# Kernel optimization log

Measured on AMD Instinct MI355X. Metric: run time of the kernel, lower is better.

The kernel has to match this reference:

```python
import jax, jax.numpy as jnp
import numpy as np

B, C_MAX, T = 128, 272, 512
D1 = 320
NUM_SUBJECTS = 8
NUM_CHANNELS = [272, 256, 240, 224, 208, 270, 260, 248]


def setup_inputs() -> dict:
    key = jax.random.key(0)
    k_x, k_w, k_s = jax.random.split(key, 3)
    X = jax.random.normal(k_x, (B, C_MAX, T), dtype=jnp.float32)
    subject_idxs = jax.random.randint(k_s, (B,), 0, NUM_SUBJECTS)
    # Per-subject Conv1d(kernel=1, bias=False) weights, padded to C_MAX.
    # Original module only reads the first num_channels[s] input channels;
    # zeroing the padded columns reproduces that exactly.
    W = jax.random.normal(k_w, (NUM_SUBJECTS, D1, C_MAX), dtype=jnp.float32) * 0.02
    mask = np.zeros((NUM_SUBJECTS, 1, C_MAX), dtype=np.float32)
    for s, nc in enumerate(NUM_CHANNELS):
        mask[s, 0, :nc] = 1.0
    W = W * jnp.asarray(mask)
    return {"X": X, "subject_idxs": subject_idxs, "W": W}


def reference(X, subject_idxs, W):
    # Gather per-sample weight matrix [B, D1, C_MAX] by subject id, then
    # batched 1x1 conv == matmul over channels at every time step.
    Wsel = W[subject_idxs]                      # [B, D1, C]
    out = jnp.einsum("bdc,bct->bdt", Wsel, X)   # [B, D1, T]
    return out
```

## Files before the change

### kernel.cpp

```cpp
#include <hip/hip_runtime.h>

#define BB    128
#define CC    272
#define TT    512
#define DD1   320
#define KC    32
#define NCHUNK 9
#define NT    64
#define MT    160
#define LDA   40
#define LDB2  66

typedef float  f32x4  __attribute__((ext_vector_type(4)));
typedef __bf16 bf16x4 __attribute__((ext_vector_type(4)));
typedef __bf16 bf16x8 __attribute__((ext_vector_type(8)));

#define BAR() asm volatile("s_waitcnt lgkmcnt(0)\ns_barrier" ::: "memory")

__global__ __launch_bounds__(256, 4)
void subj_conv_mfma(const float* __restrict__ X,
                    const int*   __restrict__ sidx,
                    const float* __restrict__ W,
                    float*       __restrict__ out) {
    const int b  = blockIdx.x;
    const int T0 = blockIdx.y * NT;
    const int d0 = blockIdx.z * MT;
    const int s  = sidx[b];

    __shared__ __bf16 As[2][MT * LDA];
    __shared__ float  Bs[2][KC * LDB2];

    const int tid  = threadIdx.x;
    const int lane = tid & 63;
    const int wv   = tid >> 6;
    const int wm   = wv & 1;
    const int wn   = wv >> 1;
    const int quad = lane >> 4;
    const int l16  = lane & 15;

    const float* Wb = W + ((size_t)s * DD1 + d0) * CC;
    const float* Xb = X + (size_t)b * CC * TT + T0;

    const int am  = tid >> 3;
    const int akk = (tid & 7) * 4;
    const int bcr = tid >> 4;
    const int bt  = (tid & 15) * 4;

    f32x4 acc[5][2];
#pragma unroll
    for (int mt = 0; mt < 5; ++mt) {
        acc[mt][0] = (f32x4){0.f, 0.f, 0.f, 0.f};
        acc[mt][1] = (f32x4){0.f, 0.f, 0.f, 0.f};
    }

    float4 pa[5];
    float4 pb[2];

    auto load_chunk = [&](int c0) {
#pragma unroll
        for (int p = 0; p < 5; ++p) {
            const int m = am + 32 * p;
            const int c = c0 + akk;
            float4 v = make_float4(0.f, 0.f, 0.f, 0.f);
            if (c < CC) v = *(const float4*)(Wb + (size_t)m * CC + c);
            pa[p] = v;
        }
#pragma unroll
        for (int p = 0; p < 2; ++p) {
            const int c = c0 + bcr + 16 * p;
            float4 v = make_float4(0.f, 0.f, 0.f, 0.f);
            if (c < CC) v = *(const float4*)(Xb + (size_t)c * TT + bt);
            pb[p] = v;
        }
    };

    auto store_chunk = [&](int buf) {
#pragma unroll
        for (int p = 0; p < 5; ++p) {
            const int m = am + 32 * p;
            bf16x4 h = {(__bf16)pa[p].x, (__bf16)pa[p].y,
                        (__bf16)pa[p].z, (__bf16)pa[p].w};
            *(bf16x4*)&As[buf][m * LDA + akk] = h;
        }
#pragma unroll
        for (int p = 0; p < 2; ++p) {
            const int cr = bcr + 16 * p;
            float* row = &Bs[buf][cr * LDB2 + bt];
            *(float2*)(row + 0) = make_float2(pb[p].x, pb[p].y);
            *(float2*)(row + 2) = make_float2(pb[p].z, pb[p].w);
        }
    };

    load_chunk(0);
    store_chunk(0);
    load_chunk(KC);
    BAR();

    for (int kc = 0; kc < NCHUNK; ++kc) {
        const int cur = kc & 1;

        bf16x8 bfr[2];
#pragma unroll
        for (int nt = 0; nt < 2; ++nt) {
            const int tcol = wn * 32 + nt * 16 + l16;
            bf16x8 h;
#pragma unroll
            for (int j = 0; j < 8; ++j)
                h[j] = (__bf16)Bs[cur][(quad * 8 + j) * LDB2 + tcol];
            bfr[nt] = h;
        }

#pragma unroll
        for (int mt = 0; mt < 5; ++mt) {
            bf16x8 af = *(const bf16x8*)&As[cur][(wm * 80 + mt * 16 + l16) * LDA + quad * 8];
#pragma unroll
            for (int nt = 0; nt < 2; ++nt)
                acc[mt][nt] = __builtin_amdgcn_mfma_f32_16x16x32_bf16(
                    af, bfr[nt], acc[mt][nt], 0, 0, 0);
        }

        if (kc + 1 < NCHUNK) {
            store_chunk(1 - cur);
            if (kc + 2 < NCHUNK) load_chunk((kc + 2) * KC);
            BAR();
        }
    }

#pragma unroll
    for (int mt = 0; mt < 5; ++mt) {
        const int d = d0 + wm * 80 + mt * 16 + quad * 4;
#pragma unroll
        for (int nt = 0; nt < 2; ++nt) {
            float* ob = out + ((size_t)b * DD1 + d) * TT + T0 + wn * 32 + nt * 16 + l16;
#pragma unroll
            for (int r = 0; r < 4; ++r)
                ob[(size_t)r * TT] = acc[mt][nt][r];
        }
    }
}

extern "C" void kernel_launch(void* const* d_in, const int* in_sizes, int n_in,
                              void* d_out, int out_size, void* d_ws, size_t ws_size,
                              hipStream_t stream) {
    const float* X    = (const float*)d_in[0];
    const int*   sidx = (const int*)  d_in[1];
    const float* W    = (const float*)d_in[2];
    float*       out  = (float*)d_out;

    dim3 grid(BB, TT / NT, 2);
    dim3 block(256);
    subj_conv_mfma<<<grid, block, 0, stream>>>(X, sidx, W, out);
}
```

Measured before the change: 164.5 us.

## Store X tile transposed as bf16 in LDS for vector fragment reads

```diff
diff --git a/kernel.cpp b/kernel.cpp
--- a/kernel.cpp
+++ b/kernel.cpp
@@ -9,7 +9,7 @@
 #define NT    64
 #define MT    160
 #define LDA   40
-#define LDB2  66
+#define LDBT  40
 
 typedef float  f32x4  __attribute__((ext_vector_type(4)));
 typedef __bf16 bf16x4 __attribute__((ext_vector_type(4)));
@@ -27,8 +27,8 @@
     const int d0 = blockIdx.z * MT;
     const int s  = sidx[b];
 
-    __shared__ __bf16 As[2][MT * LDA];
-    __shared__ float  Bs[2][KC * LDB2];
+    __shared__ __align__(16) __bf16 As[2][MT * LDA];
+    __shared__ __align__(16) __bf16 Bs[2][NT * LDBT];
 
     const int tid  = threadIdx.x;
     const int lane = tid & 63;
@@ -43,8 +43,7 @@
 
     const int am  = tid >> 3;
     const int akk = (tid & 7) * 4;
-    const int bcr = tid >> 4;
-    const int bt  = (tid & 15) * 4;
+    const float* Xc = Xb + (size_t)(8 * wv) * TT + lane;
 
     f32x4 acc[5][2];
 #pragma unroll
@@ -54,46 +53,48 @@
     }
 
     float4 pa[5];
-    float4 pb[2];
+    float  pbx[8];
 
-    auto load_chunk = [&](int c0) {
+    auto load_chunk_full = [&](int c0) {
+#pragma unroll
+        for (int p = 0; p < 5; ++p)
+            pa[p] = *(const float4*)(Wb + (size_t)(am + 32 * p) * CC + c0 + akk);
+#pragma unroll
+        for (int r = 0; r < 8; ++r)
+            pbx[r] = Xc[(size_t)(c0 + r) * TT];
+    };
+
+    auto load_chunk_guard = [&](int c0) {
 #pragma unroll
         for (int p = 0; p < 5; ++p) {
-            const int m = am + 32 * p;
             const int c = c0 + akk;
             float4 v = make_float4(0.f, 0.f, 0.f, 0.f);
-            if (c < CC) v = *(const float4*)(Wb + (size_t)m * CC + c);
+            if (c < CC) v = *(const float4*)(Wb + (size_t)(am + 32 * p) * CC + c);
             pa[p] = v;
         }
 #pragma unroll
-        for (int p = 0; p < 2; ++p) {
-            const int c = c0 + bcr + 16 * p;
-            float4 v = make_float4(0.f, 0.f, 0.f, 0.f);
-            if (c < CC) v = *(const float4*)(Xb + (size_t)c * TT + bt);
-            pb[p] = v;
+        for (int r = 0; r < 8; ++r) {
+            const int c = c0 + 8 * wv + r;
+            pbx[r] = (c < CC) ? Xc[(size_t)(c0 + r) * TT] : 0.f;
         }
     };
 
     auto store_chunk = [&](int buf) {
 #pragma unroll
         for (int p = 0; p < 5; ++p) {
-            const int m = am + 32 * p;
             bf16x4 h = {(__bf16)pa[p].x, (__bf16)pa[p].y,
                         (__bf16)pa[p].z, (__bf16)pa[p].w};
-            *(bf16x4*)&As[buf][m * LDA + akk] = h;
+            *(bf16x4*)&As[buf][(am + 32 * p) * LDA + akk] = h;
         }
+        bf16x8 hb;
 #pragma unroll
-        for (int p = 0; p < 2; ++p) {
-            const int cr = bcr + 16 * p;
-            float* row = &Bs[buf][cr * LDB2 + bt];
-            *(float2*)(row + 0) = make_float2(pb[p].x, pb[p].y);
-            *(float2*)(row + 2) = make_float2(pb[p].z, pb[p].w);
-        }
+        for (int r = 0; r < 8; ++r) hb[r] = (__bf16)pbx[r];
+        *(bf16x8*)&Bs[buf][lane * LDBT + 8 * wv] = hb;
     };
 
-    load_chunk(0);
+    load_chunk_full(0);
     store_chunk(0);
-    load_chunk(KC);
+    load_chunk_full(KC);
     BAR();
 
     for (int kc = 0; kc < NCHUNK; ++kc) {
@@ -101,14 +102,8 @@
 
         bf16x8 bfr[2];
 #pragma unroll
-        for (int nt = 0; nt < 2; ++nt) {
-            const int tcol = wn * 32 + nt * 16 + l16;
-            bf16x8 h;
-#pragma unroll
-            for (int j = 0; j < 8; ++j)
-                h[j] = (__bf16)Bs[cur][(quad * 8 + j) * LDB2 + tcol];
-            bfr[nt] = h;
-        }
+        for (int nt = 0; nt < 2; ++nt)
+            bfr[nt] = *(const bf16x8*)&Bs[cur][(wn * 32 + nt * 16 + l16) * LDBT + quad * 8];
 
 #pragma unroll
         for (int mt = 0; mt < 5; ++mt) {
@@ -121,7 +116,11 @@
 
         if (kc + 1 < NCHUNK) {
             store_chunk(1 - cur);
-            if (kc + 2 < NCHUNK) load_chunk((kc + 2) * KC);
+            if (kc + 2 < NCHUNK) {
+                const int c0 = (kc + 2) * KC;
+                if (kc + 2 == NCHUNK - 1) load_chunk_guard(c0);
+                else                      load_chunk_full(c0);
+            }
             BAR();
         }
     }
```

Result: slower. 184.2 us (+12.0%).

## Stage epilogue through LDS for vector stores and remap block order

Applied to the files above, without the earlier changes.

```diff
diff --git a/kernel.cpp b/kernel.cpp
--- a/kernel.cpp
+++ b/kernel.cpp
@@ -10,25 +10,29 @@
 #define MT    160
 #define LDA   40
 #define LDB2  66
+#define LDE   20
 
 typedef float  f32x4  __attribute__((ext_vector_type(4)));
 typedef __bf16 bf16x4 __attribute__((ext_vector_type(4)));
 typedef __bf16 bf16x8 __attribute__((ext_vector_type(8)));
 
 #define BAR() asm volatile("s_waitcnt lgkmcnt(0)\ns_barrier" ::: "memory")
+#define LGKM0() asm volatile("s_waitcnt lgkmcnt(0)" ::: "memory")
 
 __global__ __launch_bounds__(256, 4)
 void subj_conv_mfma(const float* __restrict__ X,
                     const int*   __restrict__ sidx,
                     const float* __restrict__ W,
                     float*       __restrict__ out) {
-    const int b  = blockIdx.x;
-    const int T0 = blockIdx.y * NT;
-    const int d0 = blockIdx.z * MT;
-    const int s  = sidx[b];
+    const int bid  = blockIdx.x;
+    const int b    = (bid & 7) + 8 * (bid >> 7);
+    const int tile = (bid >> 3) & 15;
+    const int T0   = (tile >> 1) * NT;
+    const int d0   = (tile & 1) * MT;
+    const int s    = sidx[b];
 
-    __shared__ __bf16 As[2][MT * LDA];
-    __shared__ float  Bs[2][KC * LDB2];
+    __shared__ __align__(16) __bf16 As[2][MT * LDA];
+    __shared__ __align__(16) float  Bs[2][KC * LDB2];
 
     const int tid  = threadIdx.x;
     const int lane = tid & 63;
@@ -126,15 +130,23 @@
         }
     }
 
+    BAR();
+    float* tw = (float*)As + wv * (5 * 16 * LDE);
 #pragma unroll
-    for (int mt = 0; mt < 5; ++mt) {
-        const int d = d0 + wm * 80 + mt * 16 + quad * 4;
+    for (int nt = 0; nt < 2; ++nt) {
+        if (nt) LGKM0();
 #pragma unroll
-        for (int nt = 0; nt < 2; ++nt) {
-            float* ob = out + ((size_t)b * DD1 + d) * TT + T0 + wn * 32 + nt * 16 + l16;
+        for (int mt = 0; mt < 5; ++mt)
 #pragma unroll
             for (int r = 0; r < 4; ++r)
-                ob[(size_t)r * TT] = acc[mt][nt][r];
+                tw[mt * (16 * LDE) + (quad * 4 + r) * LDE + l16] = acc[mt][nt][r];
+        LGKM0();
+#pragma unroll
+        for (int mt = 0; mt < 5; ++mt) {
+            f32x4 v = *(const f32x4*)&tw[mt * (16 * LDE) + l16 * LDE + quad * 4];
+            float* op = out + ((size_t)b * DD1 + d0 + wm * 80 + mt * 16 + l16) * TT
+                            + T0 + wn * 32 + nt * 16 + quad * 4;
+            *(f32x4*)op = v;
         }
     }
 }
@@ -147,7 +159,7 @@
     const float* W    = (const float*)d_in[2];
     float*       out  = (float*)d_out;
 
-    dim3 grid(BB, TT / NT, 2);
+    dim3 grid(BB * (TT / NT) * 2);
     dim3 block(256);
     subj_conv_mfma<<<grid, block, 0, stream>>>(X, sidx, W, out);
 }
```

New measurement: 172.2 us. 4.7% more time.

## Single-buffer LDS, raise occupancy target, and remap grid for batch-group locality

Applied to the files above, without the earlier changes.

```diff
diff --git a/kernel.cpp b/kernel.cpp
--- a/kernel.cpp
+++ b/kernel.cpp
@@ -17,18 +17,20 @@
 
 #define BAR() asm volatile("s_waitcnt lgkmcnt(0)\ns_barrier" ::: "memory")
 
-__global__ __launch_bounds__(256, 4)
+__global__ __launch_bounds__(256, 6)
 void subj_conv_mfma(const float* __restrict__ X,
                     const int*   __restrict__ sidx,
                     const float* __restrict__ W,
                     float*       __restrict__ out) {
-    const int b  = blockIdx.x;
-    const int T0 = blockIdx.y * NT;
-    const int d0 = blockIdx.z * MT;
-    const int s  = sidx[b];
+    const int bid  = blockIdx.x;
+    const int b    = (bid & 7) + 8 * (bid >> 7);
+    const int tile = (bid >> 3) & 15;
+    const int T0   = (tile >> 1) * NT;
+    const int d0   = (tile & 1) * MT;
+    const int s    = sidx[b];
 
-    __shared__ __bf16 As[2][MT * LDA];
-    __shared__ float  Bs[2][KC * LDB2];
+    __shared__ __align__(16) __bf16 As[MT * LDA];
+    __shared__ __align__(16) float  Bs[KC * LDB2];
 
     const int tid  = threadIdx.x;
     const int lane = tid & 63;
@@ -74,31 +76,24 @@
         }
     };
 
-    auto store_chunk = [&](int buf) {
+    auto store_chunk = [&]() {
 #pragma unroll
         for (int p = 0; p < 5; ++p) {
             const int m = am + 32 * p;
             bf16x4 h = {(__bf16)pa[p].x, (__bf16)pa[p].y,
                         (__bf16)pa[p].z, (__bf16)pa[p].w};
-            *(bf16x4*)&As[buf][m * LDA + akk] = h;
+            *(bf16x4*)&As[m * LDA + akk] = h;
         }
 #pragma unroll
         for (int p = 0; p < 2; ++p) {
             const int cr = bcr + 16 * p;
-            float* row = &Bs[buf][cr * LDB2 + bt];
+            float* row = &Bs[cr * LDB2 + bt];
             *(float2*)(row + 0) = make_float2(pb[p].x, pb[p].y);
             *(float2*)(row + 2) = make_float2(pb[p].z, pb[p].w);
         }
     };
 
-    load_chunk(0);
-    store_chunk(0);
-    load_chunk(KC);
-    BAR();
-
-    for (int kc = 0; kc < NCHUNK; ++kc) {
-        const int cur = kc & 1;
-
+    auto compute = [&]() {
         bf16x8 bfr[2];
 #pragma unroll
         for (int nt = 0; nt < 2; ++nt) {
@@ -106,21 +101,29 @@
             bf16x8 h;
 #pragma unroll
             for (int j = 0; j < 8; ++j)
-                h[j] = (__bf16)Bs[cur][(quad * 8 + j) * LDB2 + tcol];
+                h[j] = (__bf16)Bs[(quad * 8 + j) * LDB2 + tcol];
             bfr[nt] = h;
         }
-
 #pragma unroll
         for (int mt = 0; mt < 5; ++mt) {
-            bf16x8 af = *(const bf16x8*)&As[cur][(wm * 80 + mt * 16 + l16) * LDA + quad * 8];
+            bf16x8 af = *(const bf16x8*)&As[(wm * 80 + mt * 16 + l16) * LDA + quad * 8];
 #pragma unroll
             for (int nt = 0; nt < 2; ++nt)
                 acc[mt][nt] = __builtin_amdgcn_mfma_f32_16x16x32_bf16(
                     af, bfr[nt], acc[mt][nt], 0, 0, 0);
         }
+    };
 
+    load_chunk(0);
+    store_chunk();
+    load_chunk(KC);
+    BAR();
+
+    for (int kc = 0; kc < NCHUNK; ++kc) {
+        compute();
         if (kc + 1 < NCHUNK) {
-            store_chunk(1 - cur);
+            BAR();
+            store_chunk();
             if (kc + 2 < NCHUNK) load_chunk((kc + 2) * KC);
             BAR();
         }
@@ -147,7 +150,7 @@
     const float* W    = (const float*)d_in[2];
     float*       out  = (float*)d_out;
 
-    dim3 grid(BB, TT / NT, 2);
+    dim3 grid(BB * (TT / NT) * 2);
     dim3 block(256);
     subj_conv_mfma<<<grid, block, 0, stream>>>(X, sidx, W, out);
 }
```

Result: slower. 352.8 us (+114.4%).
